# Kernel tuning notes

Measured on AMD Instinct MI355X. Metric: run time of the kernel, lower is better.

The kernel has to match this reference:

```python
import jax, jax.numpy as jnp
import numpy as np

B, C, H, W = 4, 128, 64, 64
NUM_HEADS = 4
HEAD_DIM = C // NUM_HEADS


def setup_inputs() -> dict:
    key = jax.random.key(0)
    ks = jax.random.split(key, 9)
    s = 0.02
    return {
        "x": jax.random.normal(ks[0], (B, C, H, W), dtype=jnp.float32),
        "wq": jax.random.normal(ks[1], (C, C), dtype=jnp.float32) * s,
        "bq": jax.random.normal(ks[2], (C,), dtype=jnp.float32) * s,
        "wk": jax.random.normal(ks[3], (C, C), dtype=jnp.float32) * s,
        "bk": jax.random.normal(ks[4], (C,), dtype=jnp.float32) * s,
        "wv": jax.random.normal(ks[5], (C, C), dtype=jnp.float32) * s,
        "bv": jax.random.normal(ks[6], (C,), dtype=jnp.float32) * s,
        "wo": jax.random.normal(ks[7], (C, C), dtype=jnp.float32) * s,
        "bo": jax.random.normal(ks[8], (C,), dtype=jnp.float32) * s,
    }


def _proj(w, b, xf):
    # 1x1 conv == channel-mixing linear: xf is (B, C, N)
    return jnp.einsum("oc,bcn->bon", w, xf) + b[None, :, None]


def reference(x, wq, bq, wk, bk, wv, bv, wo, bo):
    b, c, h, w = x.shape
    n = h * w
    nh, hd = NUM_HEADS, HEAD_DIM
    xf = x.reshape(b, c, n)
    q = _proj(wq, bq, xf).reshape(b, nh, hd, n)
    k = _proj(wk, bk, xf).reshape(b, nh, hd, n)
    v = _proj(wv, bv, xf).reshape(b, nh, hd, n)
    # scores: (b, heads, n, n)
    scores = jnp.einsum("bhdn,bhdm->bhnm", q, k) / jnp.sqrt(jnp.float32(hd)).astype(x.dtype)
    prob = jax.nn.softmax(scores, axis=-1)
    # attn_out: (b, heads, head_dim, n)
    attn = jnp.einsum("bhnm,bhdm->bhdn", prob, v).reshape(b, c, n)
    out = _proj(wo, bo, attn).reshape(b, c, h, w)
    return x + out
```

## Files before the change

kernel.cpp:

```cpp
#include <hip/hip_runtime.h>
#include <hip/hip_bf16.h>

#define BB 4
#define CC 128
#define NN 4096
#define NHEAD 4
#define HDIM 32
#define KSPLIT 2

typedef short bf16x8_t __attribute__((ext_vector_type(8)));
typedef float f32x4_t __attribute__((ext_vector_type(4)));
typedef int i32x4_t __attribute__((ext_vector_type(4)));

#define MFMA16(a, b, c) __builtin_amdgcn_mfma_f32_16x16x32_bf16(a, b, c, 0, 0, 0)
#define EXP2(x) __builtin_amdgcn_exp2f(x)

#define QSCALE (0.17677669529663687f * 1.4426950408889634f)

static __device__ inline unsigned short f2bf(float f) {
  unsigned u = __builtin_bit_cast(unsigned, f);
  u += 0x7fffu + ((u >> 16) & 1u);
  return (unsigned short)(u >> 16);
}
static __device__ inline unsigned pk2(float lo, float hi) {
  return (unsigned)f2bf(lo) | ((unsigned)f2bf(hi) << 16);
}
static __device__ inline unsigned pack_trunc(float lo, float hi) {
  return __builtin_amdgcn_perm(__builtin_bit_cast(unsigned, hi),
                               __builtin_bit_cast(unsigned, lo), 0x07060302u);
}

static __device__ inline void gload_lds16(const unsigned short* gsrc, void* ldst) {
  __builtin_amdgcn_global_load_lds(
      (const __attribute__((address_space(1))) unsigned int*)gsrc,
      (__attribute__((address_space(3))) unsigned int*)ldst, 16, 0, 0);
}

__global__ __launch_bounds__(256) void qkv_mfma_kernel(
    const float* __restrict__ x,
    const float* __restrict__ wq, const float* __restrict__ wk,
    const float* __restrict__ wv,
    const float* __restrict__ bq, const float* __restrict__ bk,
    const float* __restrict__ bv,
    unsigned short* __restrict__ qt, unsigned short* __restrict__ kt,
    unsigned short* __restrict__ vg) {
  __shared__ __attribute__((aligned(16))) unsigned short wsb[128][136];
  __shared__ __attribute__((aligned(16))) unsigned short xsb[64][136];
  unsigned short(*vt)[66] = (unsigned short(*)[66]) & xsb[0][0];

  const int b = blockIdx.y, nt = blockIdx.x, proj = blockIdx.z;
  const int tid = threadIdx.x;

  const float* wsrc = (proj == 0) ? wq : (proj == 1) ? wk : wv;
  const float wscale = (proj == 0) ? QSCALE : 1.0f;

#pragma unroll
  for (int i = 0; i < 8; i++) {
    int f = tid + 256 * i;
    int c = f >> 4, n4 = (f & 15) * 4;
    float4 v4 = *(const float4*)(x + ((size_t)b * CC + c) * NN + nt * 64 + n4);
    xsb[n4 + 0][c] = f2bf(v4.x);
    xsb[n4 + 1][c] = f2bf(v4.y);
    xsb[n4 + 2][c] = f2bf(v4.z);
    xsb[n4 + 3][c] = f2bf(v4.w);
  }

#pragma unroll
  for (int i = 0; i < 16; i++) {
    int idx = i * 256 + tid;
    int o = idx >> 5, c4 = (idx & 31) * 4;
    float4 v4 = *(const float4*)(wsrc + (size_t)o * CC + c4);
    uint2 p;
    p.x = pk2(v4.x * wscale, v4.y * wscale);
    p.y = pk2(v4.z * wscale, v4.w * wscale);
    *(uint2*)&wsb[o][c4] = p;
  }
  __syncthreads();

  const int lane = tid & 63, w = tid >> 6;
  const int l16 = lane & 15, g = lane >> 4;
  const int nl = w * 16;
  const int ngl = nt * 64 + nl;

  bf16x8_t xf[4];
#pragma unroll
  for (int ks = 0; ks < 4; ks++)
    xf[ks] = *(const bf16x8_t*)&xsb[nl + l16][ks * 32 + g * 8];
  __syncthreads();

  const float* bias = (proj == 0) ? bq : (proj == 1) ? bk : bv;
  const float bsc = (proj == 0) ? QSCALE : 1.0f;
  unsigned short* qkdst = proj ? kt : qt;

#pragma unroll
  for (int ot = 0; ot < 8; ot++) {
    f32x4_t acc;
#pragma unroll
    for (int r = 0; r < 4; r++) acc[r] = bias[ot * 16 + g * 4 + r] * bsc;
#pragma unroll
    for (int ks = 0; ks < 4; ks++) {
      bf16x8_t wf = *(const bf16x8_t*)&wsb[ot * 16 + l16][ks * 32 + g * 8];
      acc = MFMA16(wf, xf[ks], acc);
    }
    if (proj < 2) {
      unsigned p0 = pk2(acc[0], acc[1]);
      unsigned p1 = pk2(acc[2], acc[3]);
      unsigned q0 = (unsigned)__shfl_xor((int)p0, 16);
      unsigned q1 = (unsigned)__shfl_xor((int)p1, 16);
      if ((g & 1) == 0) {
        int hh = ot >> 1, dblk = (ot & 1) * 2 + (g >> 1);
        unsigned short* dst =
            qkdst + (((size_t)(b * NHEAD + hh) * 4 + dblk) * NN + ngl + l16) * 8;
        uint4 val = make_uint4(p0, p1, q0, q1);
        *(uint4*)dst = val;
      }
    } else {
#pragma unroll
      for (int r = 0; r < 4; r++) vt[ot * 16 + g * 4 + r][nl + l16] = f2bf(acc[r]);
    }
  }

  if (proj == 2) {
    __syncthreads();
#pragma unroll
    for (int c = 0; c < 4; c++) {
      int cid = c * 256 + tid;
      int hh = cid >> 8, inner = cid & 255;
      int g2 = inner & 3, l16v = (inner >> 2) & 15, fh = inner >> 6;
      int fv = fh >> 1, half = fh & 1;
      int o = hh * 32 + half * 16 + l16v;
      int n0 = fv * 32 + g2 * 4;
      unsigned d0 = *(const unsigned*)&vt[o][n0];
      unsigned d1 = *(const unsigned*)&vt[o][n0 + 2];
      unsigned d2 = *(const unsigned*)&vt[o][n0 + 16];
      unsigned d3 = *(const unsigned*)&vt[o][n0 + 18];
      uint4 val = make_uint4(d0, d1, d2, d3);
      *(uint4*)(vg + (((size_t)(b * NHEAD + hh) * 64 + nt) * 256 + inner) * 8) = val;
    }
  }
}

__global__ __launch_bounds__(256, 4) void attn_mfma5_kernel(
    const unsigned short* __restrict__ qt, const unsigned short* __restrict__ kt,
    const unsigned short* __restrict__ vg,
    unsigned* __restrict__ opart, float* __restrict__ lpart) {
  __shared__ __attribute__((aligned(16))) unsigned short smem[2][4096];

  const int chunk = blockIdx.x & (KSPLIT - 1), nt = blockIdx.x / KSPLIT;
  const int h = blockIdx.y, b = blockIdx.z;
  const int bh = b * NHEAD + h;
  const int tid = threadIdx.x, lane = tid & 63, wid = tid >> 6;
  const int l16 = lane & 15, g = lane >> 4;
  const int nbase = nt * 128 + wid * 32;

  const unsigned short* qb = qt + (size_t)bh * NN * HDIM;
  const unsigned short* kb = kt + (size_t)bh * NN * HDIM;
  const unsigned short* vgb = vg + (size_t)bh * 64 * 2048;

  const bf16x8_t qf0 = *(const bf16x8_t*)(qb + ((size_t)g * NN + nbase + l16) * 8);
  const bf16x8_t qf1 = *(const bf16x8_t*)(qb + ((size_t)g * NN + nbase + 16 + l16) * 8);

  f32x4_t o00 = {0, 0, 0, 0}, o01 = {0, 0, 0, 0};
  f32x4_t o10 = {0, 0, 0, 0}, o11 = {0, 0, 0, 0};
  f32x4_t la = {0, 0, 0, 0}, lb = {0, 0, 0, 0};
  const f32x4_t zf = {0, 0, 0, 0};
  const i32x4_t onesi = {0x3F803F80, 0x3F803F80, 0x3F803F80, 0x3F803F80};
  const bf16x8_t ones = __builtin_bit_cast(bf16x8_t, onesi);

  const int NITER = 64 / KSPLIT;
  const int mt0 = chunk * NITER;

  const unsigned short* ksrc = kb + ((size_t)g * NN + mt0 * 64 + wid * 16 + l16) * 8;
  const unsigned short* vsrc = vgb + (size_t)mt0 * 2048 + (size_t)((wid * 16 + l16) * 4 + g) * 8;

  auto stage = [&](int p, int i) {
    gload_lds16(ksrc + (size_t)i * 512, &smem[p][wid * 512]);
    gload_lds16(vsrc + (size_t)i * 2048, &smem[p][2048 + wid * 512]);
  };

  auto body = [&](int p) {
    const unsigned short* sk = &smem[p][0];
    bf16x8_t k0 = *(const bf16x8_t*)(sk + 0 * 512 + lane * 8);
    bf16x8_t k1 = *(const bf16x8_t*)(sk + 1 * 512 + lane * 8);
    bf16x8_t k2 = *(const bf16x8_t*)(sk + 2 * 512 + lane * 8);
    bf16x8_t k3 = *(const bf16x8_t*)(sk + 3 * 512 + lane * 8);
    bf16x8_t vf0 = *(const bf16x8_t*)(sk + 2048 + 0 * 512 + lane * 8);
    bf16x8_t vf2 = *(const bf16x8_t*)(sk + 2048 + 1 * 512 + lane * 8);
    bf16x8_t vf1 = *(const bf16x8_t*)(sk + 2048 + 2 * 512 + lane * 8);
    bf16x8_t vf3 = *(const bf16x8_t*)(sk + 2048 + 3 * 512 + lane * 8);

    __builtin_amdgcn_s_setprio(1);
    f32x4_t sA0 = MFMA16(k0, qf0, zf), sA1 = MFMA16(k1, qf0, zf);
    f32x4_t sA2 = MFMA16(k2, qf0, zf), sA3 = MFMA16(k3, qf0, zf);
    f32x4_t sB0 = MFMA16(k0, qf1, zf), sB1 = MFMA16(k1, qf1, zf);
    f32x4_t sB2 = MFMA16(k2, qf1, zf), sB3 = MFMA16(k3, qf1, zf);
    __builtin_amdgcn_s_setprio(0);

#pragma unroll
    for (int r = 0; r < 4; r++) {
      sA0[r] = EXP2(sA0[r]); sA1[r] = EXP2(sA1[r]);
      sA2[r] = EXP2(sA2[r]); sA3[r] = EXP2(sA3[r]);
      sB0[r] = EXP2(sB0[r]); sB1[r] = EXP2(sB1[r]);
      sB2[r] = EXP2(sB2[r]); sB3[r] = EXP2(sB3[r]);
    }

    i32x4_t pA0i = {(int)pack_trunc(sA0[0], sA0[1]), (int)pack_trunc(sA0[2], sA0[3]),
                    (int)pack_trunc(sA1[0], sA1[1]), (int)pack_trunc(sA1[2], sA1[3])};
    i32x4_t pA1i = {(int)pack_trunc(sA2[0], sA2[1]), (int)pack_trunc(sA2[2], sA2[3]),
                    (int)pack_trunc(sA3[0], sA3[1]), (int)pack_trunc(sA3[2], sA3[3])};
    i32x4_t pB0i = {(int)pack_trunc(sB0[0], sB0[1]), (int)pack_trunc(sB0[2], sB0[3]),
                    (int)pack_trunc(sB1[0], sB1[1]), (int)pack_trunc(sB1[2], sB1[3])};
    i32x4_t pB1i = {(int)pack_trunc(sB2[0], sB2[1]), (int)pack_trunc(sB2[2], sB2[3]),
                    (int)pack_trunc(sB3[0], sB3[1]), (int)pack_trunc(sB3[2], sB3[3])};
    bf16x8_t pA0 = __builtin_bit_cast(bf16x8_t, pA0i);
    bf16x8_t pA1 = __builtin_bit_cast(bf16x8_t, pA1i);
    bf16x8_t pB0 = __builtin_bit_cast(bf16x8_t, pB0i);
    bf16x8_t pB1 = __builtin_bit_cast(bf16x8_t, pB1i);

    __builtin_amdgcn_s_setprio(1);
    o00 = MFMA16(vf0, pA0, o00); o00 = MFMA16(vf1, pA1, o00);
    o01 = MFMA16(vf2, pA0, o01); o01 = MFMA16(vf3, pA1, o01);
    o10 = MFMA16(vf0, pB0, o10); o10 = MFMA16(vf1, pB1, o10);
    o11 = MFMA16(vf2, pB0, o11); o11 = MFMA16(vf3, pB1, o11);

    la = MFMA16(ones, pA0, la); la = MFMA16(ones, pA1, la);
    lb = MFMA16(ones, pB0, lb); lb = MFMA16(ones, pB1, lb);
    __builtin_amdgcn_s_setprio(0);
  };

  stage(0, 0);
  __syncthreads();
  for (int mi = 0; mi < NITER; mi += 2) {
    stage(1, mi + 1);
    body(0);
    __syncthreads();
    if (mi + 2 < NITER) stage(0, mi + 2);
    body(1);
    __syncthreads();
  }

  unsigned* ob32 = opart + ((size_t)(chunk * BB * NHEAD + bh)) * HDIM * (NN / 2);
  const int wnd16 = (nbase >> 5) * 16;
#pragma unroll
  for (int r = 0; r < 4; r++) {
    ob32[(size_t)(g * 4 + r) * (NN / 2) + wnd16 + l16] = pk2(o00[r], o10[r]);
    ob32[(size_t)(16 + g * 4 + r) * (NN / 2) + wnd16 + l16] = pk2(o01[r], o11[r]);
  }
  if (g == 0) {
    float* lb_ = lpart + (size_t)(chunk * BB * NHEAD + bh) * NN;
    lb_[nbase + l16] = la[0];
    lb_[nbase + 16 + l16] = lb[0];
  }
}

__global__ __launch_bounds__(512) void out_mfma_kernel(
    const unsigned* __restrict__ opart, const float* __restrict__ lpart,
    const float* __restrict__ wo, const float* __restrict__ bo,
    const float* __restrict__ x, float* __restrict__ out) {
  __shared__ __attribute__((aligned(16))) unsigned short wsb[128][136];
  __shared__ __attribute__((aligned(16))) unsigned short xsb[64][136];
  __shared__ float linv[NHEAD][64];
  const int b = blockIdx.y, nt = blockIdx.x;
  const int tid = threadIdx.x;

#pragma unroll
  for (int i = 0; i < 8; i++) {
    int idx = i * 512 + tid;
    int o = idx >> 5, c4 = (idx & 31) * 4;
    float4 v4 = *(const float4*)(wo + (size_t)o * CC + c4);
    uint2 p;
    p.x = pk2(v4.x, v4.y);
    p.y = pk2(v4.z, v4.w);
    *(uint2*)&wsb[o][c4] = p;
  }

  if (tid < 256) {
    int h = tid >> 6, nn = tid & 63;
    int bh = b * NHEAD + h;
    float l = 0.f;
#pragma unroll
    for (int c = 0; c < KSPLIT; c++)
      l += lpart[(size_t)(c * BB * NHEAD + bh) * NN + nt * 64 + nn];
    linv[h][nn] = 1.f / l;
  }
  __syncthreads();

  const size_t ROWD = NN / 2;
  const size_t CH32 = (size_t)BB * NHEAD * HDIM * ROWD;
  const unsigned* obb = opart + (size_t)b * NHEAD * HDIM * ROWD;
#pragma unroll
  for (int i = 0; i < 2; i++) {
    int s = i * 512 + tid;
    int cd = s >> 3, q = s & 7;
    size_t a = (size_t)cd * ROWD + nt * 32 + q * 4;
    uint4 u0 = *(const uint4*)(obb + a);
    uint4 u1 = *(const uint4*)(obb + CH32 + a);
    int nb = (q >> 2) * 32 + (q & 3) * 4;
    const float* li = &linv[cd >> 5][0];
    const unsigned* w0 = (const unsigned*)&u0;
    const unsigned* w1 = (const unsigned*)&u1;
#pragma unroll
    for (int e = 0; e < 4; e++) {
      float lo = __builtin_bit_cast(float, w0[e] << 16) +
                 __builtin_bit_cast(float, w1[e] << 16);
      float hi = __builtin_bit_cast(float, w0[e] & 0xFFFF0000u) +
                 __builtin_bit_cast(float, w1[e] & 0xFFFF0000u);
      int nl = nb + e;
      xsb[nl][cd] = f2bf(lo * li[nl]);
      xsb[nl + 16][cd] = f2bf(hi * li[nl + 16]);
    }
  }
  __syncthreads();

  const int lane = tid & 63, w = tid >> 6;
  const int l16 = lane & 15, g = lane >> 4;
  const int nsub = (w & 3) * 16, mtbase = (w >> 2) * 4;
  const int n0 = nt * 64 + nsub;

  bf16x8_t bfr[4];
#pragma unroll
  for (int ks = 0; ks < 4; ks++)
    bfr[ks] = *(const bf16x8_t*)&xsb[nsub + l16][ks * 32 + g * 8];

#pragma unroll
  for (int mi = 0; mi < 4; mi++) {
    int mt = mtbase + mi;
    f32x4_t acc;
#pragma unroll
    for (int r = 0; r < 4; r++) acc[r] = bo[mt * 16 + g * 4 + r];
#pragma unroll
    for (int ks = 0; ks < 4; ks++) {
      bf16x8_t af = *(const bf16x8_t*)&wsb[mt * 16 + l16][ks * 32 + g * 8];
      acc = MFMA16(af, bfr[ks], acc);
    }
#pragma unroll
    for (int r = 0; r < 4; r++) {
      int o = mt * 16 + g * 4 + r;
      size_t addr = ((size_t)b * CC + o) * NN + n0 + l16;
      out[addr] = acc[r] + x[addr];
    }
  }
}

extern "C" void kernel_launch(void* const* d_in, const int* in_sizes, int n_in,
                              void* d_out, int out_size, void* d_ws, size_t ws_size,
                              hipStream_t stream) {
  const float* x  = (const float*)d_in[0];
  const float* wq = (const float*)d_in[1];
  const float* bq = (const float*)d_in[2];
  const float* wk = (const float*)d_in[3];
  const float* bk = (const float*)d_in[4];
  const float* wv = (const float*)d_in[5];
  const float* bv = (const float*)d_in[6];
  const float* wo = (const float*)d_in[7];
  const float* bo = (const float*)d_in[8];
  float* out = (float*)d_out;

  char* w = (char*)d_ws;
  const size_t SZ = (size_t)BB * NHEAD * NN * HDIM * 2;
  unsigned short* qt    = (unsigned short*)w;
  unsigned short* kt    = (unsigned short*)(w + SZ);
  unsigned short* vg    = (unsigned short*)(w + 2 * SZ);
  unsigned* opart = (unsigned*)(w + 3 * SZ);
  float* lpart = (float*)(w + 3 * SZ +
                          (size_t)KSPLIT * BB * NHEAD * HDIM * NN * 2);

  qkv_mfma_kernel<<<dim3(NN / 64, BB, 3), 256, 0, stream>>>(
      x, wq, wk, wv, bq, bk, bv, qt, kt, vg);
  attn_mfma5_kernel<<<dim3((NN / 128) * KSPLIT, NHEAD, BB), 256, 0, stream>>>(
      qt, kt, vg, opart, lpart);
  out_mfma_kernel<<<dim3(NN / 64, BB), 512, 0, stream>>>(
      opart, lpart, wo, bo, x, out);
}
```

Measured before the change: 129.1 us.

## Software-pipeline QK MFMA of next tile with softmax/PV of current tile

The attention loop now computes the QK score MFMAs for tile i+1 while doing exp2, bf16 packing and PV MFMAs for tile i, using two register score sets that alternate. The LDS ring grows from double to quadruple buffering, so K/V loads are issued two tiles ahead. The aim is to hide exp/pack VALU latency behind matrix-core work and to hide load latency better. In exchange, register pressure roughly doubles for scores and LDS use doubles, which is why the launch bound drops from 4 to 3 blocks per CU and may lower occupancy.

```diff
diff --git a/kernel.cpp b/kernel.cpp
--- a/kernel.cpp
+++ b/kernel.cpp
@@ -140,11 +140,11 @@
   }
 }
 
-__global__ __launch_bounds__(256, 4) void attn_mfma5_kernel(
+__global__ __launch_bounds__(256, 3) void attn_mfma5_kernel(
     const unsigned short* __restrict__ qt, const unsigned short* __restrict__ kt,
     const unsigned short* __restrict__ vg,
     unsigned* __restrict__ opart, float* __restrict__ lpart) {
-  __shared__ __attribute__((aligned(16))) unsigned short smem[2][4096];
+  __shared__ __attribute__((aligned(16))) unsigned short smem[4][4096];
 
   const int chunk = blockIdx.x & (KSPLIT - 1), nt = blockIdx.x / KSPLIT;
   const int h = blockIdx.y, b = blockIdx.z;
@@ -178,40 +178,43 @@
     gload_lds16(vsrc + (size_t)i * 2048, &smem[p][2048 + wid * 512]);
   };
 
-  auto body = [&](int p) {
+  f32x4_t Sx[8], Sy[8];
+
+  auto qk = [&](int p, f32x4_t (&S)[8]) {
     const unsigned short* sk = &smem[p][0];
     bf16x8_t k0 = *(const bf16x8_t*)(sk + 0 * 512 + lane * 8);
     bf16x8_t k1 = *(const bf16x8_t*)(sk + 1 * 512 + lane * 8);
     bf16x8_t k2 = *(const bf16x8_t*)(sk + 2 * 512 + lane * 8);
     bf16x8_t k3 = *(const bf16x8_t*)(sk + 3 * 512 + lane * 8);
-    bf16x8_t vf0 = *(const bf16x8_t*)(sk + 2048 + 0 * 512 + lane * 8);
-    bf16x8_t vf2 = *(const bf16x8_t*)(sk + 2048 + 1 * 512 + lane * 8);
-    bf16x8_t vf1 = *(const bf16x8_t*)(sk + 2048 + 2 * 512 + lane * 8);
-    bf16x8_t vf3 = *(const bf16x8_t*)(sk + 2048 + 3 * 512 + lane * 8);
-
     __builtin_amdgcn_s_setprio(1);
-    f32x4_t sA0 = MFMA16(k0, qf0, zf), sA1 = MFMA16(k1, qf0, zf);
-    f32x4_t sA2 = MFMA16(k2, qf0, zf), sA3 = MFMA16(k3, qf0, zf);
-    f32x4_t sB0 = MFMA16(k0, qf1, zf), sB1 = MFMA16(k1, qf1, zf);
-    f32x4_t sB2 = MFMA16(k2, qf1, zf), sB3 = MFMA16(k3, qf1, zf);
+    S[0] = MFMA16(k0, qf0, zf); S[1] = MFMA16(k1, qf0, zf);
+    S[2] = MFMA16(k2, qf0, zf); S[3] = MFMA16(k3, qf0, zf);
+    S[4] = MFMA16(k0, qf1, zf); S[5] = MFMA16(k1, qf1, zf);
+    S[6] = MFMA16(k2, qf1, zf); S[7] = MFMA16(k3, qf1, zf);
     __builtin_amdgcn_s_setprio(0);
-
-#pragma unroll
-    for (int r = 0; r < 4; r++) {
-      sA0[r] = EXP2(sA0[r]); sA1[r] = EXP2(sA1[r]);
-      sA2[r] = EXP2(sA2[r]); sA3[r] = EXP2(sA3[r]);
-      sB0[r] = EXP2(sB0[r]); sB1[r] = EXP2(sB1[r]);
-      sB2[r] = EXP2(sB2[r]); sB3[r] = EXP2(sB3[r]);
-    }
-
-    i32x4_t pA0i = {(int)pack_trunc(sA0[0], sA0[1]), (int)pack_trunc(sA0[2], sA0[3]),
-                    (int)pack_trunc(sA1[0], sA1[1]), (int)pack_trunc(sA1[2], sA1[3])};
-    i32x4_t pA1i = {(int)pack_trunc(sA2[0], sA2[1]), (int)pack_trunc(sA2[2], sA2[3]),
-                    (int)pack_trunc(sA3[0], sA3[1]), (int)pack_trunc(sA3[2], sA3[3])};
-    i32x4_t pB0i = {(int)pack_trunc(sB0[0], sB0[1]), (int)pack_trunc(sB0[2], sB0[3]),
-                    (int)pack_trunc(sB1[0], sB1[1]), (int)pack_trunc(sB1[2], sB1[3])};
-    i32x4_t pB1i = {(int)pack_trunc(sB2[0], sB2[1]), (int)pack_trunc(sB2[2], sB2[3]),
-                    (int)pack_trunc(sB3[0], sB3[1]), (int)pack_trunc(sB3[2], sB3[3])};
+  };
+
+  auto rest = [&](int p, f32x4_t (&S)[8]) {
+    const unsigned short* sv = &smem[p][2048];
+    bf16x8_t vf0 = *(const bf16x8_t*)(sv + 0 * 512 + lane * 8);
+    bf16x8_t vf2 = *(const bf16x8_t*)(sv + 1 * 512 + lane * 8);
+    bf16x8_t vf1 = *(const bf16x8_t*)(sv + 2 * 512 + lane * 8);
+    bf16x8_t vf3 = *(const bf16x8_t*)(sv + 3 * 512 + lane * 8);
+
+#pragma unroll
+    for (int j = 0; j < 8; j++) {
+#pragma unroll
+      for (int r = 0; r < 4; r++) S[j][r] = EXP2(S[j][r]);
+    }
+
+    i32x4_t pA0i = {(int)pack_trunc(S[0][0], S[0][1]), (int)pack_trunc(S[0][2], S[0][3]),
+                    (int)pack_trunc(S[1][0], S[1][1]), (int)pack_trunc(S[1][2], S[1][3])};
+    i32x4_t pA1i = {(int)pack_trunc(S[2][0], S[2][1]), (int)pack_trunc(S[2][2], S[2][3]),
+                    (int)pack_trunc(S[3][0], S[3][1]), (int)pack_trunc(S[3][2], S[3][3])};
+    i32x4_t pB0i = {(int)pack_trunc(S[4][0], S[4][1]), (int)pack_trunc(S[4][2], S[4][3]),
+                    (int)pack_trunc(S[5][0], S[5][1]), (int)pack_trunc(S[5][2], S[5][3])};
+    i32x4_t pB1i = {(int)pack_trunc(S[6][0], S[6][1]), (int)pack_trunc(S[6][2], S[6][3]),
+                    (int)pack_trunc(S[7][0], S[7][1]), (int)pack_trunc(S[7][2], S[7][3])};
     bf16x8_t pA0 = __builtin_bit_cast(bf16x8_t, pA0i);
     bf16x8_t pA1 = __builtin_bit_cast(bf16x8_t, pA1i);
     bf16x8_t pB0 = __builtin_bit_cast(bf16x8_t, pB0i);
@@ -229,15 +232,23 @@
   };
 
   stage(0, 0);
-  __syncthreads();
-  for (int mi = 0; mi < NITER; mi += 2) {
-    stage(1, mi + 1);
-    body(0);
+  stage(1, 1);
+  __syncthreads();
+  qk(0, Sx);
+
+  for (int mi = 0; mi < NITER - 2; mi += 2) {
+    stage((mi + 2) & 3, mi + 2);
+    qk((mi + 1) & 3, Sy);
+    rest(mi & 3, Sx);
     __syncthreads();
-    if (mi + 2 < NITER) stage(0, mi + 2);
-    body(1);
+    if (mi + 3 < NITER) stage((mi + 3) & 3, mi + 3);
+    qk((mi + 2) & 3, Sx);
+    rest((mi + 1) & 3, Sy);
     __syncthreads();
   }
+  qk((NITER - 1) & 3, Sy);
+  rest((NITER - 2) & 3, Sx);
+  rest((NITER - 1) & 3, Sy);
 
   unsigned* ob32 = opart + ((size_t)(chunk * BB * NHEAD + bh)) * HDIM * (NN / 2);
   const int wnd16 = (nbase >> 5) * 16;
```

New measurement: 131.2 us. No clear change (+1.6%).
